# Kernel tuning notes

Measured on AMD Instinct MI355X. Metric: run time of the kernel, lower is better.

## Reference

```python
import jax, jax.numpy as jnp
import numpy as np

STRIDE = 1  # conv stride from __init__


def setup_inputs() -> dict:
    key = jax.random.key(0)
    k1, k2, k3 = jax.random.split(key, 3)
    prot1 = jax.random.normal(k1, (4, 1024, 8, 64), dtype=jnp.float32)
    prot2 = jax.random.normal(k2, (4, 1024, 8, 64), dtype=jnp.float32)
    # W: (no_filters, no_channels, no_dims, window_size)
    W = jax.random.normal(k3, (32, 8, 64, 7), dtype=jnp.float32)
    return {"prot1": prot1, "prot2": prot2, "W": W}


def _project(x, W, stride):
    """Fused equivalent of unfold + broadcast-mul + sum over (C, window).

    x: (N, H, C, D), W: (F, C, D, w) -> (N, F, H', D) with H' = (H - w)//stride + 1.
    This is a grouped 1D conv: D groups, each mixing C input channels into F outputs.
    """
    N, H, C, D = x.shape
    Fn, _, _, w = W.shape
    xg = jnp.transpose(x, (0, 3, 2, 1)).reshape(N, D * C, H)        # (N, D*C, H)
    Wg = jnp.transpose(W, (2, 0, 1, 3)).reshape(D * Fn, C, w)       # (D*F, C, w)
    out = jax.lax.conv_general_dilated(
        xg, Wg, window_strides=(stride,), padding='VALID',
        dimension_numbers=('NCH', 'OIH', 'NCH'), feature_group_count=D)
    Hp = out.shape[-1]
    return jnp.transpose(out.reshape(N, D, Fn, Hp), (0, 2, 3, 1))   # (N, F, H', D)


def reference(prot1, prot2, W):
    q1 = _project(prot1, W, STRIDE)   # (N, F, H1', D)
    q2 = _project(prot2, W, STRIDE)   # (N, F, H2', D)
    H1p, H2p = q1.shape[2], q2.shape[2]
    scale = jnp.sqrt(jnp.asarray(H1p * H2p, dtype=q1.dtype))
    att = jnp.einsum('nfhd,nfgd->nfhg', q1, q2) / scale             # (N, F, H1', H2')
    a = jax.nn.softmax(att, axis=3)
    p1 = jnp.einsum('nfhg,nfgd->nfhd', a, q2)                       # (N, F, H1', D)
    # NB: source does transpose(att, 2, 2) (a no-op) and multiplies the SAME
    # softmax matrix by the UPDATED p1folds; we reproduce that faithfully.
    p2 = jnp.einsum('nfhg,nfgd->nfhd', a, p1)                       # (N, F, H1', D)
    out1 = jnp.tanh(jnp.transpose(p1, (0, 2, 1, 3)))                # (N, H1', F, D)
    out2 = jnp.tanh(jnp.transpose(p2, (0, 2, 1, 3)))
    # Dropout is identity in eval mode (and dropout_p=0.0 here).
    return (out1, out2)
```

## Files before the change

kernel.cpp:

```cpp
#include <hip/hip_runtime.h>
#include <math.h>

typedef __bf16 bf16_t;
typedef bf16_t bf16x4 __attribute__((ext_vector_type(4)));
typedef bf16_t bf16x8 __attribute__((ext_vector_type(8)));
typedef float  f32x16 __attribute__((ext_vector_type(16)));

#define HH 1024
#define CC 8
#define DD 64
#define FF 32
#define WW 7
#define HP 1018
#define HPAD 1024
#define NF 128
#define QOUT (NF*HP*DD)
#define QWS ((size_t)NF*HPAD*DD)

#if __has_builtin(__builtin_amdgcn_exp2f)
#define EXP2(x) __builtin_amdgcn_exp2f(x)
#else
#define EXP2(x) __expf((x) * 0.6931471805599453f)
#endif

#define QSCALE (1.442695040888963f / 1018.f)

__device__ __forceinline__ int vaddr(int row, int col) {
    return row*64 + ((((col>>3) ^ (row&7) ^ ((row>>2)&7)))<<3) + (col&7);
}

__global__ __launch_bounds__(256) void wprep_kernel(
    const float* __restrict__ Wt, float* __restrict__ Wp)
{
    const int idx = blockIdx.x * 256 + threadIdx.x;
    if (idx < FF*CC*DD*WW) {
        const int j = idx % WW;
        int t = idx / WW;
        const int d = t % DD; t /= DD;
        const int c = t % CC;
        const int f = t / CC;
        Wp[((f*CC + c)*WW + j)*DD + d] = Wt[idx];
    }
}

__global__ __launch_bounds__(256, 3) void conv_kernel(
    const float* __restrict__ x1, const float* __restrict__ x2,
    const float* __restrict__ Wp, bf16_t* __restrict__ q1, bf16_t* __restrict__ q2)
{
    __shared__ float xs[22*512];
    const int zin = blockIdx.z & 1;
    const int fh = blockIdx.z >> 1;
    const float* x = zin ? x2 : x1;
    bf16_t* q = zin ? q2 : q1;
    const float qs = zin ? 1.f : QSCALE;
    const int n = blockIdx.y;
    const int hb = blockIdx.x * 16;
    const int tid = threadIdx.x;

    const float4* xg = (const float4*)(x + (size_t)n*HH*512);
    float4* xsv = (float4*)xs;
#pragma unroll
    for (int it = 0; it < 11; ++it) {
        const int i = it*256 + tid;
        const int row = hb + (i >> 7);
        float4 v = {0.f, 0.f, 0.f, 0.f};
        if (row < HH) v = xg[(size_t)row*128 + (i & 127)];
        xsv[i] = v;
    }

    const int d = tid & 63;
    const int fq = tid >> 6;

    float w[2][CC][WW];
#pragma unroll
    for (int fi = 0; fi < 2; ++fi) {
        const int f = fq*8 + fh*2 + fi;
#pragma unroll
        for (int c = 0; c < CC; ++c)
#pragma unroll
            for (int j = 0; j < WW; ++j)
                w[fi][c][j] = Wp[((f*CC + c)*WW + j)*DD + d];
    }

    __syncthreads();

    float acc[2][16];
#pragma unroll
    for (int fi = 0; fi < 2; ++fi)
#pragma unroll
        for (int i = 0; i < 16; ++i) acc[fi][i] = 0.f;

#pragma unroll
    for (int rr = 0; rr < 22; ++rr) {
        float xv[CC];
#pragma unroll
        for (int c = 0; c < CC; ++c)
            xv[c] = xs[rr*512 + c*64 + d];
#pragma unroll
        for (int fi = 0; fi < 2; ++fi)
#pragma unroll
            for (int j = 0; j < WW; ++j) {
                const int i = rr - j;
                if (i >= 0 && i < 16) {
#pragma unroll
                    for (int c = 0; c < CC; ++c)
                        acc[fi][i] = fmaf(xv[c], w[fi][c][j], acc[fi][i]);
                }
            }
    }

#pragma unroll
    for (int fi = 0; fi < 2; ++fi) {
        const int f = fq*8 + fh*2 + fi;
#pragma unroll
        for (int i = 0; i < 16; ++i) {
            const int h = hb + i;
            const float v = (h < HP) ? acc[fi][i]*qs : 0.f;
            q[((size_t)(n*FF + f)*HPAD + h)*DD + d] = (bf16_t)v;
        }
    }
}

__device__ __forceinline__ float fast_tanh(float x) {
    const float t = __expf(2.f * x);
    return (t - 1.f) / (t + 1.f);
}

#define S_PHASE(Cd, aqm) {                                                        \
    f32x16 _z{};                                                                  \
    Cd[0] = _z; Cd[1] = _z;                                                       \
    __builtin_amdgcn_s_setprio(1);                                                \
    _Pragma("unroll")                                                             \
    for (int kt = 0; kt < 4; ++kt) {                                              \
        Cd[0] = __builtin_amdgcn_mfma_f32_32x32x16_bf16(aqm[kt], bq1[0][kt], Cd[0], 0,0,0); \
        Cd[1] = __builtin_amdgcn_mfma_f32_32x32x16_bf16(aqm[kt], bq1[1][kt], Cd[1], 0,0,0); \
    }                                                                             \
    __builtin_amdgcn_s_setprio(0); }

#define EXP_PHASE(Cs, af, mtv) {                                                  \
    _Pragma("unroll")                                                             \
    for (int nt = 0; nt < 2; ++nt) {                                              \
        float ls = 0.f;                                                           \
        _Pragma("unroll")                                                         \
        for (int s = 0; s < 16; ++s) {                                            \
            float e = EXP2(Cs[nt][s]);                                            \
            if (tail) {                                                           \
                const int gg = g0 + 32*(mtv) + (s&3) + 8*(s>>2) + 4*half;         \
                if (gg >= HP) e = 0.f;                                            \
            }                                                                     \
            ls += e;                                                              \
            af[nt][s>>3][s&7] = (bf16_t)e;                                        \
        }                                                                         \
        lacc[nt] += ls;                                                           \
    } }

#define PV_PHASE(af, mtv) {                                                       \
    __builtin_amdgcn_s_setprio(1);                                                \
    _Pragma("unroll")                                                             \
    for (int u = 0; u < 2; ++u) {                                                 \
        _Pragma("unroll")                                                         \
        for (int dt = 0; dt < 2; ++dt) {                                          \
            const int chunk = (4*(mtv) + 2*u + half) ^ vswz;                      \
            bf16x8 b = *(const bf16x8*)&vtc[(32*dt + lid)*64 + chunk*8];          \
            O[0][dt] = __builtin_amdgcn_mfma_f32_32x32x16_bf16(af[0][u], b, O[0][dt], 0,0,0); \
            O[1][dt] = __builtin_amdgcn_mfma_f32_32x32x16_bf16(af[1][u], b, O[1][dt], 0,0,0); \
        }                                                                         \
    }                                                                             \
    __builtin_amdgcn_s_setprio(0); }

template<int MODE>
__global__ __launch_bounds__(256, 2) void flash(
    const bf16_t* __restrict__ q1, const bf16_t* __restrict__ q2,
    const bf16_t* __restrict__ vsrc, bf16_t* __restrict__ p1out,
    float* __restrict__ out)
{
    __shared__ __align__(16) bf16_t Vt[2][64*64];

    const int head = blockIdx.y;
    const int n = head >> 5, f = head & 31;
    const int tid = threadIdx.x;
    const int w = tid >> 6;
    const int lane = tid & 63;
    const int lid = lane & 31;
    const int half = lane >> 5;
    const int hb = blockIdx.x * 256 + w * 64;

    const size_t qoff = (size_t)head * HPAD * DD;
    const int vswz = (lid & 7) ^ (lid >> 2);

    const int gq = tid >> 4;
    const int dq = tid & 15;
    const int cgb = 4*((gq>>1)&1) + 8*(gq&1) + 16*(gq>>2);

    const bf16_t* vptr = (MODE == 1) ? vsrc : q2;

    const bf16_t* bp = q1 + qoff + (size_t)(hb + lid)*DD + 8*half;
    const bf16_t* ap = q2 + qoff + (size_t)lid*DD + 8*half;
    const bf16_t* vp = vptr + qoff + (size_t)(4*gq)*DD + 4*dq;

    bf16x8 bq1[2][4];
#pragma unroll
    for (int nt = 0; nt < 2; ++nt)
#pragma unroll
        for (int kt = 0; kt < 4; ++kt)
            bq1[nt][kt] = *(const bf16x8*)&bp[(size_t)(32*nt)*DD + 16*kt];

    bf16x8 aq[2][4];
#pragma unroll
    for (int mt = 0; mt < 2; ++mt)
#pragma unroll
        for (int kt = 0; kt < 4; ++kt)
            aq[mt][kt] = *(const bf16x8*)&ap[(size_t)(32*mt)*DD + 16*kt];

    bf16x4 rV[4];
#pragma unroll
    for (int i = 0; i < 4; ++i)
        rV[i] = *(const bf16x4*)&vp[(size_t)i*DD];
#pragma unroll
    for (int j = 0; j < 4; ++j) {
        bf16x4 c = { rV[0][j], rV[1][j], rV[2][j], rV[3][j] };
        *(bf16x4*)&Vt[0][vaddr(4*dq + j, cgb)] = c;
    }
#pragma unroll
    for (int i = 0; i < 4; ++i)
        rV[i] = *(const bf16x4*)&vp[(size_t)(64 + i)*DD];

    f32x16 O[2][2] = {};
    float lacc[2] = {0.f, 0.f};

    f32x16 CA[2], CB[2];
    S_PHASE(CA, aq[0]);
#pragma unroll
    for (int kt = 0; kt < 4; ++kt)
        aq[0][kt] = *(const bf16x8*)&ap[(size_t)64*DD + 16*kt];

    __syncthreads();

    for (int t = 0; t < 16; ++t) {
        const int g0 = t << 6;
        const bf16_t* vtc = Vt[t & 1];
        const bool tail = (t == 15);

        if (t + 1 < 16) {
            bf16_t* vtn = Vt[(t + 1) & 1];
#pragma unroll
            for (int j = 0; j < 4; ++j) {
                bf16x4 c = { rV[0][j], rV[1][j], rV[2][j], rV[3][j] };
                *(bf16x4*)&vtn[vaddr(4*dq + j, cgb)] = c;
            }
            if (t + 2 < 16) {
#pragma unroll
                for (int i = 0; i < 4; ++i)
                    rV[i] = *(const bf16x4*)&vp[(size_t)((t + 2)*64 + i)*DD];
            }
        }

        S_PHASE(CB, aq[1]);
        if (t + 1 < 16) {
#pragma unroll
            for (int kt = 0; kt < 4; ++kt)
                aq[1][kt] = *(const bf16x8*)&ap[(size_t)((t + 1)*64 + 32)*DD + 16*kt];
        }
        {
            bf16x8 af[2][2];
            EXP_PHASE(CA, af, 0);
            PV_PHASE(af, 0);
        }

        if (t + 1 < 16) {
            S_PHASE(CA, aq[0]);
            if (t + 2 < 16) {
#pragma unroll
                for (int kt = 0; kt < 4; ++kt)
                    aq[0][kt] = *(const bf16x8*)&ap[(size_t)((t + 2)*64)*DD + 16*kt];
            }
        }
        {
            bf16x8 af[2][2];
            EXP_PHASE(CB, af, 1);
            PV_PHASE(af, 1);
        }

        __syncthreads();
    }

    float linv[2];
#pragma unroll
    for (int nt = 0; nt < 2; ++nt) {
        const float l = lacc[nt] + __shfl_xor(lacc[nt], 32);
        linv[nt] = 1.f / l;
    }
#pragma unroll
    for (int ht = 0; ht < 2; ++ht) {
#pragma unroll
        for (int s = 0; s < 16; ++s) {
            const int R = (s&3) + 8*(s>>2) + 4*half;
            const float li = __shfl(linv[ht], R);
            const int hg = hb + 32*ht + R;
#pragma unroll
            for (int dt = 0; dt < 2; ++dt) {
                const int d = 32*dt + lid;
                const float val = O[ht][dt][s] * li;
                if (hg < HP)
                    out[(((size_t)n*HP + hg)*FF + f)*DD + d] = fast_tanh(val);
                if (MODE == 0)
                    p1out[qoff + (size_t)hg*DD + d] = (bf16_t)(hg < HP ? val : 0.f);
            }
        }
    }
}

extern "C" void kernel_launch(void* const* d_in, const int* in_sizes, int n_in,
                              void* d_out, int out_size, void* d_ws, size_t ws_size,
                              hipStream_t stream)
{
    const float* prot1 = (const float*)d_in[0];
    const float* prot2 = (const float*)d_in[1];
    const float* Wt    = (const float*)d_in[2];
    float* out = (float*)d_out;

    bf16_t* q1b = (bf16_t*)d_ws;
    bf16_t* q2b = q1b + QWS;
    bf16_t* p1b = q2b + QWS;
    float* Wp   = (float*)(p1b + QWS);

    wprep_kernel<<<dim3(448), 256, 0, stream>>>(Wt, Wp);
    conv_kernel<<<dim3(64, 4, 8), 256, 0, stream>>>(prot1, prot2, Wp, q1b, q2b);
    flash<0><<<dim3(4, NF), 256, 0, stream>>>(q1b, q2b, q2b, p1b, out);
    flash<1><<<dim3(4, NF), 256, 0, stream>>>(q1b, q2b, p1b, p1b, out + QOUT);
}
```

Before: 209.1 us.

## Replace software-pipelined S/exp/PV schedule with per-warp staggered order

Removes the explicit software pipeline that overlapped the next QK^T MFMA block with the current exp and PV phases, and replaces it with a sequential MT_STEP (QK, exp, PV) per 32-row subtile. Odd and even warps process the two subtiles in opposite order, so different waves are in MFMA-heavy and exp-heavy phases at the same time, using cross-wave rather than in-wave overlap. This frees the second score accumulator set, lowering register pressure, but gives up the in-wave latency hiding of the old schedule.

```diff
diff --git a/kernel.cpp b/kernel.cpp
--- a/kernel.cpp
+++ b/kernel.cpp
@@ -126,24 +126,27 @@
     return (t - 1.f) / (t + 1.f);
 }
 
-#define S_PHASE(Cd, aqm) {                                                        \
-    f32x16 _z{};                                                                  \
-    Cd[0] = _z; Cd[1] = _z;                                                       \
+#define MT_STEP(mtv) {                                                            \
+    f32x16 C[2] = {};                                                             \
     __builtin_amdgcn_s_setprio(1);                                                \
     _Pragma("unroll")                                                             \
     for (int kt = 0; kt < 4; ++kt) {                                              \
-        Cd[0] = __builtin_amdgcn_mfma_f32_32x32x16_bf16(aqm[kt], bq1[0][kt], Cd[0], 0,0,0); \
-        Cd[1] = __builtin_amdgcn_mfma_f32_32x32x16_bf16(aqm[kt], bq1[1][kt], Cd[1], 0,0,0); \
+        C[0] = __builtin_amdgcn_mfma_f32_32x32x16_bf16(aq[mtv][kt], bq1[0][kt], C[0], 0,0,0); \
+        C[1] = __builtin_amdgcn_mfma_f32_32x32x16_bf16(aq[mtv][kt], bq1[1][kt], C[1], 0,0,0); \
     }                                                                             \
-    __builtin_amdgcn_s_setprio(0); }
-
-#define EXP_PHASE(Cs, af, mtv) {                                                  \
+    __builtin_amdgcn_s_setprio(0);                                                \
+    if (g0 + 64 < HPAD) {                                                         \
+        _Pragma("unroll")                                                         \
+        for (int kt = 0; kt < 4; ++kt)                                            \
+            aq[mtv][kt] = *(const bf16x8*)&ap[(size_t)(g0 + 64 + 32*(mtv))*DD + 16*kt]; \
+    }                                                                             \
+    bf16x8 af[2][2];                                                              \
     _Pragma("unroll")                                                             \
     for (int nt = 0; nt < 2; ++nt) {                                              \
         float ls = 0.f;                                                           \
         _Pragma("unroll")                                                         \
         for (int s = 0; s < 16; ++s) {                                            \
-            float e = EXP2(Cs[nt][s]);                                            \
+            float e = EXP2(C[nt][s]);                                             \
             if (tail) {                                                           \
                 const int gg = g0 + 32*(mtv) + (s&3) + 8*(s>>2) + 4*half;         \
                 if (gg >= HP) e = 0.f;                                            \
@@ -152,9 +155,7 @@
             af[nt][s>>3][s&7] = (bf16_t)e;                                        \
         }                                                                         \
         lacc[nt] += ls;                                                           \
-    } }
-
-#define PV_PHASE(af, mtv) {                                                       \
+    }                                                                             \
     __builtin_amdgcn_s_setprio(1);                                                \
     _Pragma("unroll")                                                             \
     for (int u = 0; u < 2; ++u) {                                                 \
@@ -184,6 +185,7 @@
     const int lid = lane & 31;
     const int half = lane >> 5;
     const int hb = blockIdx.x * 256 + w * 64;
+    const bool odd = ((w ^ blockIdx.x ^ blockIdx.y) & 1) != 0;
 
     const size_t qoff = (size_t)head * HPAD * DD;
     const int vswz = (lid & 7) ^ (lid >> 2);
@@ -228,18 +230,11 @@
     f32x16 O[2][2] = {};
     float lacc[2] = {0.f, 0.f};
 
-    f32x16 CA[2], CB[2];
-    S_PHASE(CA, aq[0]);
-#pragma unroll
-    for (int kt = 0; kt < 4; ++kt)
-        aq[0][kt] = *(const bf16x8*)&ap[(size_t)64*DD + 16*kt];
-
     __syncthreads();
 
     for (int t = 0; t < 16; ++t) {
         const int g0 = t << 6;
         const bf16_t* vtc = Vt[t & 1];
-        const bool tail = (t == 15);
 
         if (t + 1 < 16) {
             bf16_t* vtn = Vt[(t + 1) & 1];
@@ -255,31 +250,10 @@
             }
         }
 
-        S_PHASE(CB, aq[1]);
-        if (t + 1 < 16) {
-#pragma unroll
-            for (int kt = 0; kt < 4; ++kt)
-                aq[1][kt] = *(const bf16x8*)&ap[(size_t)((t + 1)*64 + 32)*DD + 16*kt];
-        }
-        {
-            bf16x8 af[2][2];
-            EXP_PHASE(CA, af, 0);
-            PV_PHASE(af, 0);
-        }
-
-        if (t + 1 < 16) {
-            S_PHASE(CA, aq[0]);
-            if (t + 2 < 16) {
-#pragma unroll
-                for (int kt = 0; kt < 4; ++kt)
-                    aq[0][kt] = *(const bf16x8*)&ap[(size_t)((t + 2)*64)*DD + 16*kt];
-            }
-        }
-        {
-            bf16x8 af[2][2];
-            EXP_PHASE(CB, af, 1);
-            PV_PHASE(af, 1);
-        }
+        const bool tail = (g0 + 64 > HP);
+
+        if (odd) { MT_STEP(1); MT_STEP(0); }
+        else     { MT_STEP(0); MT_STEP(1); }
 
         __syncthreads();
     }
```

Result: no change. 208.6 us (-0.2%).
